# Performance work log

Measured on AMD Instinct MI355X. Metric: run time of the kernel, lower is better.

The kernel has to match this reference:

```python
import jax, jax.numpy as jnp
import numpy as np

BS, SEQ, INP, HID = 64, 512, 512, 1024

def setup_inputs() -> dict:
    key = jax.random.key(0)
    k1, k2, k3, k4, k5 = jax.random.split(key, 5)
    scale_ih = 1.0 / np.sqrt(HID)
    return {
        "x_in": jax.random.normal(k1, (BS, SEQ, INP), dtype=jnp.float32),
        "W_ih": jax.random.normal(k2, (HID, INP), dtype=jnp.float32) * scale_ih,
        "W_hh": jax.random.normal(k3, (HID, HID), dtype=jnp.float32) * scale_ih,
        "b_ih": jax.random.normal(k4, (HID,), dtype=jnp.float32) * scale_ih,
        "b_hh": jax.random.normal(k5, (HID,), dtype=jnp.float32) * scale_ih,
    }

def reference(x_in, W_ih, W_hh, b_ih, b_hh):
    # batch_first=True: x_in is (B, S, F); permute to (S, B, F)
    x = jnp.swapaxes(x_in, 0, 1)
    # Precompute input projection for all timesteps in one big GEMM: (S, B, H)
    xw = jnp.einsum('sbf,hf->sbh', x, W_ih) + b_ih + b_hh
    h0 = jnp.zeros((x_in.shape[0], W_hh.shape[0]), dtype=x_in.dtype)

    def step(h, xt):
        # RNNCell: h' = tanh(x W_ih^T + b_ih + h W_hh^T + b_hh)
        h_new = jnp.tanh(xt + h @ W_hh.T)
        return h_new, h_new

    _, hiddens = jax.lax.scan(step, h0, xw)  # (S, B, H)
    return jnp.swapaxes(hiddens, 0, 1)  # back to (B, S, H)
```

## Files before the change

### kernel.cpp

```cpp
#include <hip/hip_runtime.h>

#define BATCH 64
#define SEQ   512
#define INP   512
#define HID   1024
#define MAGIC 0x13570000u

__global__ __launch_bounds__(256) void xw_gemm(
    const float* __restrict__ X, const float* __restrict__ Wih,
    const float* __restrict__ bih, const float* __restrict__ bhh,
    float* __restrict__ out)
{
    __shared__ float As[8][128];
    __shared__ float Bs[8][128];
    const int t  = threadIdx.x;
    const int m0 = blockIdx.x * 128;
    const int n0 = blockIdx.y * 128;
    const int lr = t >> 1;
    const int lk = (t & 1) * 4;
    const int ty = t >> 4;
    const int tx = t & 15;

    float acc[8][8];
#pragma unroll
    for (int i = 0; i < 8; ++i)
#pragma unroll
        for (int j = 0; j < 8; ++j) acc[i][j] = 0.f;

    const float* xrow = X   + (size_t)(m0 + lr) * INP + lk;
    const float* wrow = Wih + (size_t)(n0 + lr) * INP + lk;

    for (int k0 = 0; k0 < INP; k0 += 8) {
        float4 av = *(const float4*)(xrow + k0);
        float4 bv = *(const float4*)(wrow + k0);
        __syncthreads();
        As[lk + 0][lr] = av.x; As[lk + 1][lr] = av.y;
        As[lk + 2][lr] = av.z; As[lk + 3][lr] = av.w;
        Bs[lk + 0][lr] = bv.x; Bs[lk + 1][lr] = bv.y;
        Bs[lk + 2][lr] = bv.z; Bs[lk + 3][lr] = bv.w;
        __syncthreads();
#pragma unroll
        for (int kk = 0; kk < 8; ++kk) {
            float4 a0 = *(const float4*)&As[kk][ty * 4];
            float4 a1 = *(const float4*)&As[kk][64 + ty * 4];
            float4 b0 = *(const float4*)&Bs[kk][tx * 4];
            float4 b1 = *(const float4*)&Bs[kk][64 + tx * 4];
            float am[8] = {a0.x, a0.y, a0.z, a0.w, a1.x, a1.y, a1.z, a1.w};
            float bn[8] = {b0.x, b0.y, b0.z, b0.w, b1.x, b1.y, b1.z, b1.w};
#pragma unroll
            for (int i = 0; i < 8; ++i)
#pragma unroll
                for (int j = 0; j < 8; ++j)
                    acc[i][j] = fmaf(am[i], bn[j], acc[i][j]);
        }
    }

    const int nA = n0 + tx * 4;
    const int nB = n0 + 64 + tx * 4;
    float4 bA1 = *(const float4*)(bih + nA);
    float4 bA2 = *(const float4*)(bhh + nA);
    float4 bB1 = *(const float4*)(bih + nB);
    float4 bB2 = *(const float4*)(bhh + nB);
    float4 biasA = make_float4(bA1.x + bA2.x, bA1.y + bA2.y, bA1.z + bA2.z, bA1.w + bA2.w);
    float4 biasB = make_float4(bB1.x + bB2.x, bB1.y + bB2.y, bB1.z + bB2.z, bB1.w + bB2.w);

#pragma unroll
    for (int i = 0; i < 8; ++i) {
        int mloc = (i < 4) ? (ty * 4 + i) : (64 + ty * 4 + (i - 4));
        size_t m = (size_t)(m0 + mloc);
        float4 vA = make_float4(acc[i][0] + biasA.x, acc[i][1] + biasA.y,
                                acc[i][2] + biasA.z, acc[i][3] + biasA.w);
        float4 vB = make_float4(acc[i][4] + biasB.x, acc[i][5] + biasB.y,
                                acc[i][6] + biasB.z, acc[i][7] + biasB.w);
        *(float4*)(out + m * HID + nA) = vA;
        *(float4*)(out + m * HID + nB) = vB;
    }
}

__global__ __launch_bounds__(256) void rnn_scan(
    const float* __restrict__ Whh, float* __restrict__ out,
    unsigned* __restrict__ flags)
{
    __shared__ float4 Wlds[16][256];

    const int t  = threadIdx.x;
    const int g  = blockIdx.x >> 6;
    const int jt = blockIdx.x & 63;

    {
        const int r  = t >> 4;
        const int cb = t & 15;
        const float4* src = (const float4*)(Whh + (size_t)(jt * 16 + r) * HID);
#pragma unroll
        for (int i = 0; i < 16; ++i) {
            int c4 = i * 16 + cb;
            Wlds[r][(c4 + r) & 255] = src[c4];
        }
    }

    const int lane = t & 63;
    const int wv   = t >> 6;
    const int kc   = lane >> 4;
    const int jl   = lane & 15;
    const int bb   = g * 16 + wv * 4;

    __syncthreads();

    for (int s = 0; s < SEQ; ++s) {
        float a0 = 0.f, a1 = 0.f, a2 = 0.f, a3 = 0.f;

        if (s > 0) {
            if (t < 64) {
                const unsigned want = MAGIC + (unsigned)(s - 1);
                unsigned* f = flags + ((((s - 1) & 7) * 4 + g) * 64 + t);
                while (__hip_atomic_load(f, __ATOMIC_RELAXED, __HIP_MEMORY_SCOPE_AGENT) != want)
                    __builtin_amdgcn_s_sleep(1);
            }
            __syncthreads();
            __builtin_amdgcn_fence(__ATOMIC_ACQUIRE, "agent");

            const float4* h0 = (const float4*)(out + ((size_t)(bb + 0) * SEQ + (s - 1)) * HID);
            const float4* h1 = (const float4*)(out + ((size_t)(bb + 1) * SEQ + (s - 1)) * HID);
            const float4* h2 = (const float4*)(out + ((size_t)(bb + 2) * SEQ + (s - 1)) * HID);
            const float4* h3 = (const float4*)(out + ((size_t)(bb + 3) * SEQ + (s - 1)) * HID);

#pragma unroll 4
            for (int i = 0; i < 64; ++i) {
                const int L = kc * 64 + i;
                const float4 w4 = Wlds[jl][(L + jl) & 255];
                const float4 x0 = h0[L];
                const float4 x1 = h1[L];
                const float4 x2 = h2[L];
                const float4 x3 = h3[L];
                a0 = fmaf(x0.x, w4.x, a0); a0 = fmaf(x0.y, w4.y, a0);
                a0 = fmaf(x0.z, w4.z, a0); a0 = fmaf(x0.w, w4.w, a0);
                a1 = fmaf(x1.x, w4.x, a1); a1 = fmaf(x1.y, w4.y, a1);
                a1 = fmaf(x1.z, w4.z, a1); a1 = fmaf(x1.w, w4.w, a1);
                a2 = fmaf(x2.x, w4.x, a2); a2 = fmaf(x2.y, w4.y, a2);
                a2 = fmaf(x2.z, w4.z, a2); a2 = fmaf(x2.w, w4.w, a2);
                a3 = fmaf(x3.x, w4.x, a3); a3 = fmaf(x3.y, w4.y, a3);
                a3 = fmaf(x3.z, w4.z, a3); a3 = fmaf(x3.w, w4.w, a3);
            }
            a0 += __shfl_xor(a0, 16); a0 += __shfl_xor(a0, 32);
            a1 += __shfl_xor(a1, 16); a1 += __shfl_xor(a1, 32);
            a2 += __shfl_xor(a2, 16); a2 += __shfl_xor(a2, 32);
            a3 += __shfl_xor(a3, 16); a3 += __shfl_xor(a3, 32);
        }

        if (lane < 16) {
            const int j = jt * 16 + jl;
            float* p0 = out + ((size_t)(bb + 0) * SEQ + s) * HID + j;
            float* p1 = out + ((size_t)(bb + 1) * SEQ + s) * HID + j;
            float* p2 = out + ((size_t)(bb + 2) * SEQ + s) * HID + j;
            float* p3 = out + ((size_t)(bb + 3) * SEQ + s) * HID + j;
            float v0 = tanhf(*p0 + a0);
            float v1 = tanhf(*p1 + a1);
            float v2 = tanhf(*p2 + a2);
            float v3 = tanhf(*p3 + a3);
            __hip_atomic_store(p0, v0, __ATOMIC_RELAXED, __HIP_MEMORY_SCOPE_AGENT);
            __hip_atomic_store(p1, v1, __ATOMIC_RELAXED, __HIP_MEMORY_SCOPE_AGENT);
            __hip_atomic_store(p2, v2, __ATOMIC_RELAXED, __HIP_MEMORY_SCOPE_AGENT);
            __hip_atomic_store(p3, v3, __ATOMIC_RELAXED, __HIP_MEMORY_SCOPE_AGENT);
        }
        __syncthreads();
        if (t == 0)
            __hip_atomic_store(flags + (((s & 7) * 4 + g) * 64 + jt),
                               MAGIC + (unsigned)s,
                               __ATOMIC_RELAXED, __HIP_MEMORY_SCOPE_AGENT);
    }
}

extern "C" void kernel_launch(void* const* d_in, const int* in_sizes, int n_in,
                              void* d_out, int out_size, void* d_ws, size_t ws_size,
                              hipStream_t stream)
{
    (void)in_sizes; (void)n_in; (void)out_size; (void)ws_size;
    const float* x   = (const float*)d_in[0];
    const float* Wih = (const float*)d_in[1];
    const float* Whh = (const float*)d_in[2];
    const float* bih = (const float*)d_in[3];
    const float* bhh = (const float*)d_in[4];
    float* out = (float*)d_out;
    unsigned* flags = (unsigned*)d_ws;

    dim3 g1(BATCH * SEQ / 128, HID / 128);
    xw_gemm<<<g1, 256, 0, stream>>>(x, Wih, bih, bhh, out);
    rnn_scan<<<256, 256, 0, stream>>>(Whh, out, flags);
}
```

Before: 8.924 ms.

## Keep W_hh slice in registers and stage hidden state through LDS

The recurrent scan kernel now holds each thread's slice of W_hh in 32 float4 registers instead of LDS. Each step it cooperatively loads the previous hidden state for its 16 batch rows from global memory into a swizzled LDS buffer, so the dot products read h from LDS rather than issuing many redundant global loads per wave. Block size doubles to 512 threads, and the xw input is prefetched at the start of each step, ahead of the flag wait. This trades register pressure (128 VGPRs for weights) and an extra barrier per step for fewer global loads on the serial critical path.

New measurement: 12.50 ms. 1.4x slower.

```diff
diff --git a/kernel.cpp b/kernel.cpp
--- a/kernel.cpp
+++ b/kernel.cpp
@@ -77,36 +77,49 @@
     }
 }
 
-__global__ __launch_bounds__(256) void rnn_scan(
+__global__ __launch_bounds__(512) void rnn_scan(
     const float* __restrict__ Whh, float* __restrict__ out,
     unsigned* __restrict__ flags)
 {
-    __shared__ float4 Wlds[16][256];
+    __shared__ float4 Hlds[16][256];
 
     const int t  = threadIdx.x;
     const int g  = blockIdx.x >> 6;
     const int jt = blockIdx.x & 63;
 
+    const int lane = t & 63;
+    const int w    = t >> 6;
+    const int bq   = w >> 1;
+    const int jh   = w & 1;
+    const int kc   = lane >> 3;
+    const int jl   = lane & 7;
+    const int row  = jh * 8 + jl;
+    const int b4   = bq * 4;
+    const int Lb   = kc * 32;
+
+    float4 wreg[32];
     {
-        const int r  = t >> 4;
-        const int cb = t & 15;
-        const float4* src = (const float4*)(Whh + (size_t)(jt * 16 + r) * HID);
-#pragma unroll
-        for (int i = 0; i < 16; ++i) {
-            int c4 = i * 16 + cb;
-            Wlds[r][(c4 + r) & 255] = src[c4];
-        }
-    }
-
-    const int lane = t & 63;
-    const int wv   = t >> 6;
-    const int kc   = lane >> 4;
-    const int jl   = lane & 15;
-    const int bb   = g * 16 + wv * 4;
+        const float4* wsrc =
+            (const float4*)(Whh + (size_t)(jt * 16 + row) * HID) + (size_t)Lb;
+#pragma unroll
+        for (int i = 0; i < 32; ++i) wreg[i] = wsrc[i];
+    }
+
+    const bool act = (lane < 32);
+    const int  q   = kc & 3;
+    float* outp = out + ((size_t)(g * 16 + b4 + q) * SEQ) * HID + (jt * 16 + row);
+
+    const float4* h0p = &Hlds[b4 + 0][Lb];
+    const float4* h1p = &Hlds[b4 + 1][Lb];
+    const float4* h2p = &Hlds[b4 + 2][Lb];
+    const float4* h3p = &Hlds[b4 + 3][Lb];
 
     __syncthreads();
 
     for (int s = 0; s < SEQ; ++s) {
+        float xwv = 0.f;
+        if (act) xwv = outp[(size_t)s * HID];
+
         float a0 = 0.f, a1 = 0.f, a2 = 0.f, a3 = 0.f;
 
         if (s > 0) {
@@ -119,19 +132,32 @@
             __syncthreads();
             __builtin_amdgcn_fence(__ATOMIC_ACQUIRE, "agent");
 
-            const float4* h0 = (const float4*)(out + ((size_t)(bb + 0) * SEQ + (s - 1)) * HID);
-            const float4* h1 = (const float4*)(out + ((size_t)(bb + 1) * SEQ + (s - 1)) * HID);
-            const float4* h2 = (const float4*)(out + ((size_t)(bb + 2) * SEQ + (s - 1)) * HID);
-            const float4* h3 = (const float4*)(out + ((size_t)(bb + 3) * SEQ + (s - 1)) * HID);
-
-#pragma unroll 4
-            for (int i = 0; i < 64; ++i) {
-                const int L = kc * 64 + i;
-                const float4 w4 = Wlds[jl][(L + jl) & 255];
-                const float4 x0 = h0[L];
-                const float4 x1 = h1[L];
-                const float4 x2 = h2[L];
-                const float4 x3 = h3[L];
+            {
+                const float* hb = out + ((size_t)(g * 16) * SEQ + (s - 1)) * HID;
+                float4 tmp[8];
+#pragma unroll
+                for (int i = 0; i < 8; ++i) {
+                    int idx = i * 512 + t;
+                    tmp[i] = *(const float4*)(hb + (size_t)(idx >> 8) * (SEQ * HID)
+                                                 + (size_t)(idx & 255) * 4);
+                }
+#pragma unroll
+                for (int i = 0; i < 8; ++i) {
+                    int idx = i * 512 + t;
+                    int c   = idx & 255;
+                    Hlds[idx >> 8][c ^ ((c >> 5) & 7)] = tmp[i];
+                }
+            }
+            __syncthreads();
+
+#pragma unroll
+            for (int i = 0; i < 32; ++i) {
+                const float4 w4 = wreg[i];
+                const int sc = i ^ kc;
+                const float4 x0 = h0p[sc];
+                const float4 x1 = h1p[sc];
+                const float4 x2 = h2p[sc];
+                const float4 x3 = h3p[sc];
                 a0 = fmaf(x0.x, w4.x, a0); a0 = fmaf(x0.y, w4.y, a0);
                 a0 = fmaf(x0.z, w4.z, a0); a0 = fmaf(x0.w, w4.w, a0);
                 a1 = fmaf(x1.x, w4.x, a1); a1 = fmaf(x1.y, w4.y, a1);
@@ -141,26 +167,17 @@
                 a3 = fmaf(x3.x, w4.x, a3); a3 = fmaf(x3.y, w4.y, a3);
                 a3 = fmaf(x3.z, w4.z, a3); a3 = fmaf(x3.w, w4.w, a3);
             }
-            a0 += __shfl_xor(a0, 16); a0 += __shfl_xor(a0, 32);
-            a1 += __shfl_xor(a1, 16); a1 += __shfl_xor(a1, 32);
-            a2 += __shfl_xor(a2, 16); a2 += __shfl_xor(a2, 32);
-            a3 += __shfl_xor(a3, 16); a3 += __shfl_xor(a3, 32);
+            a0 += __shfl_xor(a0, 8); a0 += __shfl_xor(a0, 16); a0 += __shfl_xor(a0, 32);
+            a1 += __shfl_xor(a1, 8); a1 += __shfl_xor(a1, 16); a1 += __shfl_xor(a1, 32);
+            a2 += __shfl_xor(a2, 8); a2 += __shfl_xor(a2, 16); a2 += __shfl_xor(a2, 32);
+            a3 += __shfl_xor(a3, 8); a3 += __shfl_xor(a3, 16); a3 += __shfl_xor(a3, 32);
         }
 
-        if (lane < 16) {
-            const int j = jt * 16 + jl;
-            float* p0 = out + ((size_t)(bb + 0) * SEQ + s) * HID + j;
-            float* p1 = out + ((size_t)(bb + 1) * SEQ + s) * HID + j;
-            float* p2 = out + ((size_t)(bb + 2) * SEQ + s) * HID + j;
-            float* p3 = out + ((size_t)(bb + 3) * SEQ + s) * HID + j;
-            float v0 = tanhf(*p0 + a0);
-            float v1 = tanhf(*p1 + a1);
-            float v2 = tanhf(*p2 + a2);
-            float v3 = tanhf(*p3 + a3);
-            __hip_atomic_store(p0, v0, __ATOMIC_RELAXED, __HIP_MEMORY_SCOPE_AGENT);
-            __hip_atomic_store(p1, v1, __ATOMIC_RELAXED, __HIP_MEMORY_SCOPE_AGENT);
-            __hip_atomic_store(p2, v2, __ATOMIC_RELAXED, __HIP_MEMORY_SCOPE_AGENT);
-            __hip_atomic_store(p3, v3, __ATOMIC_RELAXED, __HIP_MEMORY_SCOPE_AGENT);
+        if (act) {
+            float v = (q == 0) ? a0 : (q == 1) ? a1 : (q == 2) ? a2 : a3;
+            v = tanhf(xwv + v);
+            __hip_atomic_store(outp + (size_t)s * HID, v,
+                               __ATOMIC_RELAXED, __HIP_MEMORY_SCOPE_AGENT);
         }
         __syncthreads();
         if (t == 0)
@@ -185,5 +202,5 @@
 
     dim3 g1(BATCH * SEQ / 128, HID / 128);
     xw_gemm<<<g1, 256, 0, stream>>>(x, Wih, bih, bhh, out);
-    rnn_scan<<<256, 256, 0, stream>>>(Whh, out, flags);
+    rnn_scan<<<256, 512, 0, stream>>>(Whh, out, flags);
 }
```
